# Kernel optimization log

Measured on AMD Instinct MI355X. Metric: run time of the kernel, lower is better.

Reference implementation:

```python
import jax, jax.numpy as jnp
import numpy as np

KERNEL_MUL = 2.0
KERNEL_NUM = 5


def setup_inputs() -> dict:
    key = jax.random.key(0)
    k1, k2 = jax.random.split(key)
    N, D = 4096, 256
    source = jax.random.normal(k1, (N, D), dtype=jnp.float32)
    target = jax.random.normal(k2, (N, D), dtype=jnp.float32)
    return {"source": source, "target": target}


def _gaussian_kernel_sum(source, target):
    # total: [2N, D]
    total = jnp.concatenate([source, target], axis=0)
    n = total.shape[0]
    sq = jnp.sum(total * total, axis=1)  # [2N]
    L2 = sq[:, None] + sq[None, :] - 2.0 * (total @ total.T)  # [2N, 2N]
    # Bandwidth from detached mean of off-diagonal-normalized sum (torch uses .data)
    bandwidth = jax.lax.stop_gradient(jnp.sum(L2)) / (n * n - n)
    bandwidth = bandwidth / (KERNEL_MUL ** (KERNEL_NUM // 2))
    kernels = sum(
        jnp.exp(-L2 / (bandwidth * (KERNEL_MUL ** i))) for i in range(KERNEL_NUM)
    )
    return kernels


def reference(source, target):
    b = source.shape[0]
    K = _gaussian_kernel_sum(source, target)
    XX = jnp.mean(K[:b, :b])
    YY = jnp.mean(K[b:, b:])
    XY = jnp.mean(K[:b, b:])
    YX = jnp.mean(K[b:, :b])
    return XX + YY - XY - YX
```

## Files before the change

kernel.cpp:

```cpp
#include <hip/hip_runtime.h>


#define NROWS 8192
#define HALF  4096
#define DIM   256
#define CONVB 256
#define NTILE 2080

typedef float f32x4 __attribute__((ext_vector_type(4)));

__device__ __forceinline__ const float* row_ptr(const float* src, const float* tgt, int r) {
    return (r < HALF) ? (src + (size_t)r * DIM) : (tgt + (size_t)(r - HALF) * DIM);
}

__global__ __launch_bounds__(256) void k_conv(const float* __restrict__ src,
                                              const float* __restrict__ tgt,
                                              unsigned char* __restrict__ hi,
                                              float* __restrict__ sq,
                                              float* __restrict__ part,
                                              double* __restrict__ parts1,
                                              float* __restrict__ out) {
    __shared__ __align__(16) unsigned char sh8[32 * 256];
    __shared__ float4 cs[4][64];
    __shared__ double s1s[4];

    int w = threadIdx.x >> 6, lane = threadIdx.x & 63;
    int r0 = blockIdx.x * 32;

    float4 v[8];
    #pragma unroll
    for (int i = 0; i < 8; ++i) {
        int row = r0 + w * 8 + i;
        v[i] = ((const float4*)row_ptr(src, tgt, row))[lane];
    }

    float4 csum = {0.f, 0.f, 0.f, 0.f};
    double s1w = 0.0;
    #pragma unroll
    for (int i = 0; i < 8; ++i) {
        int rl  = w * 8 + i;
        float xs[4] = {v[i].x, v[i].y, v[i].z, v[i].w};
        int pk = __builtin_amdgcn_cvt_pk_fp8_f32(xs[0], xs[1], 0, false);
        pk     = __builtin_amdgcn_cvt_pk_fp8_f32(xs[2], xs[3], pk, true);
        int o  = lane >> 1, h = lane & 1;
        *(int*)&sh8[rl * 256 + (((o ^ rl) & 31) << 3) + (h << 2)] = pk;
        csum.x += xs[0]; csum.y += xs[1]; csum.z += xs[2]; csum.w += xs[3];
        float sf = xs[0]*xs[0] + xs[1]*xs[1] + xs[2]*xs[2] + xs[3]*xs[3];
        float q0 = __builtin_amdgcn_cvt_f32_fp8(pk, 0);
        float q1 = __builtin_amdgcn_cvt_f32_fp8(pk, 1);
        float q2 = __builtin_amdgcn_cvt_f32_fp8(pk, 2);
        float q3 = __builtin_amdgcn_cvt_f32_fp8(pk, 3);
        float sQ = q0*q0 + q1*q1 + q2*q2 + q3*q3;
        #pragma unroll
        for (int off = 32; off; off >>= 1) {
            sf += __shfl_xor(sf, off, 64);
            sQ += __shfl_xor(sQ, off, 64);
        }
        if (lane == 0) { sq[r0 + rl] = sQ; s1w += (double)sf; }
    }
    __syncthreads();
    int panel = blockIdx.x >> 2, quarter = blockIdx.x & 3;
    #pragma unroll
    for (int c = threadIdx.x; c < 512; c += 256) {
        int u = c >> 5, rl = c & 31;
        int tt = u >> 2, j = u & 3;
        int o0 = 8 * tt + j;
        int o1 = 8 * tt + 4 + j;
        unsigned long long q0 = *(const unsigned long long*)
            &sh8[rl * 256 + (((o0 ^ rl) & 31) << 3)];
        unsigned long long q1 = *(const unsigned long long*)
            &sh8[rl * 256 + (((o1 ^ rl) & 31) << 3)];
        ulonglong2 q = {q0, q1};
        size_t goff = ((size_t)panel * 2048 + (size_t)u * 128 + quarter * 32 + rl);
        ((ulonglong2*)hi)[goff] = q;
    }
    cs[w][lane] = csum;
    if (lane == 0) s1s[w] = s1w;
    __syncthreads();
    if (w == 0) {
        float4 a = cs[0][lane], b = cs[1][lane], c = cs[2][lane], d = cs[3][lane];
        float4 tot = {a.x + b.x + c.x + d.x, a.y + b.y + c.y + d.y,
                      a.z + b.z + c.z + d.z, a.w + b.w + c.w + d.w};
        *(float4*)&part[(size_t)blockIdx.x * DIM + lane * 4] = tot;
        if (lane == 0) parts1[blockIdx.x] = s1s[0] + s1s[1] + s1s[2] + s1s[3];
    }
    if (blockIdx.x == 0 && threadIdx.x == 0) out[0] = 0.0f;
}

__global__ __launch_bounds__(256) void k_scale(const double* __restrict__ parts1,
                                               const float* __restrict__ part,
                                               float* __restrict__ scale) {
    __shared__ double sh[256];
    int t = threadIdx.x;
    sh[t] = parts1[t];
    __syncthreads();
    for (int off = 128; off; off >>= 1) {
        if (t < off) sh[t] += sh[t + off];
        __syncthreads();
    }
    double S1 = sh[0];
    __syncthreads();
    float c0 = 0.f, c1 = 0.f, c2 = 0.f, c3 = 0.f;
    #pragma unroll 16
    for (int b = 0; b < CONVB; b += 4) {
        c0 += part[(b + 0) * DIM + t];
        c1 += part[(b + 1) * DIM + t];
        c2 += part[(b + 2) * DIM + t];
        c3 += part[(b + 3) * DIM + t];
    }
    double c = (double)((c0 + c1) + (c2 + c3));
    sh[t] = c * c;
    __syncthreads();
    for (int off = 128; off; off >>= 1) {
        if (t < off) sh[t] += sh[t + off];
        __syncthreads();
    }
    if (t == 0) {
        double S2    = sh[0];
        double n     = (double)NROWS;
        double sumL2 = 2.0 * n * S1 - 2.0 * S2;
        double bw    = sumL2 / (n * n - n) / 4.0;
        *scale = (float)(-1.0 / (16.0 * bw * 0.69314718055994530942));
    }
}

__global__ __launch_bounds__(256, 2) void k_pairs(const unsigned char* __restrict__ hi,
                                                  const float* __restrict__ sq,
                                                  const float* __restrict__ scale_p,
                                                  float* __restrict__ out) {
    int id = blockIdx.x;
    int I = 0;
    for (;;) {
        int cnt = 64 - I;
        if (id < cnt) break;
        id -= cnt; ++I;
    }
    int J = I + id;

    __shared__ float wsum[4];

    int t    = threadIdx.x;
    int lane = t & 63;
    int w    = t >> 6;
    int lr   = lane & 15, lq = lane >> 4;
    int wr   = w >> 1, wc = w & 1;

    float wgt = (J == I) ? 1.0f : 2.0f;
    float sgn = ((I < 32) == (J < 32)) ? 1.0f : -1.0f;

    const ulonglong2* hp = (const ulonglong2*)hi;
    const ulonglong2* pA = hp + (size_t)I * 2048 + (size_t)lq * 128 + wr * 64 + lr;
    const ulonglong2* pB = hp + (size_t)J * 2048 + (size_t)lq * 128 + wc * 64 + lr;

    f32x4 acc[4][4];
    #pragma unroll
    for (int m = 0; m < 4; ++m)
        #pragma unroll
        for (int n = 0; n < 4; ++n) acc[m][n] = (f32x4){0.f, 0.f, 0.f, 0.f};

    ulonglong2 fA[4][4], fB[4][4];
    #pragma unroll
    for (int tt = 0; tt < 4; ++tt) {
        #pragma unroll
        for (int m = 0; m < 4; ++m) fA[tt][m] = pA[tt * 512 + m * 16];
        #pragma unroll
        for (int n = 0; n < 4; ++n) fB[tt][n] = pB[tt * 512 + n * 16];
    }

    #pragma unroll
    for (int tt = 0; tt < 4; ++tt) {
        #pragma unroll
        for (int m = 0; m < 4; ++m)
            #pragma unroll
            for (int n = 0; n < 4; ++n)
                acc[m][n] = __builtin_amdgcn_mfma_f32_16x16x32_fp8_fp8(
                    (long)fA[tt][m].x, (long)fB[tt][n].x, acc[m][n], 0, 0, 0);
        #pragma unroll
        for (int m = 0; m < 4; ++m)
            #pragma unroll
            for (int n = 0; n < 4; ++n)
                acc[m][n] = __builtin_amdgcn_mfma_f32_16x16x32_fp8_fp8(
                    (long)fA[tt][m].y, (long)fB[tt][n].y, acc[m][n], 0, 0, 0);
    }

    float scale = *scale_p;
    int ro_eff = I * 128 + wr * 64;
    int co_eff = J * 128 + wc * 64;
    float4 sqa4[4];
    float  sqbv[4];
    #pragma unroll
    for (int m = 0; m < 4; ++m) sqa4[m] = *(const float4*)&sq[ro_eff + m * 16 + lq * 4];
    #pragma unroll
    for (int n = 0; n < 4; ++n) sqbv[n] = sq[co_eff + n * 16 + lr];

    float tsum = 0.0f;
    #pragma unroll
    for (int m = 0; m < 4; ++m) {
        float sa[4] = {sqa4[m].x, sqa4[m].y, sqa4[m].z, sqa4[m].w};
        #pragma unroll
        for (int n = 0; n < 4; ++n) {
            #pragma unroll
            for (int r = 0; r < 4; ++r) {
                float L2  = sa[r] + sqbv[n] - 2.0f * acc[m][n][r];
                float u   = __builtin_amdgcn_exp2f(scale * L2);
                float u2  = u * u;
                float u4  = u2 * u2;
                float u8  = u4 * u4;
                float u16 = u8 * u8;
                tsum += u + u2 + u4 + u8 + u16;
            }
        }
    }

    #pragma unroll
    for (int off = 32; off; off >>= 1) tsum += __shfl_xor(tsum, off, 64);
    if (lane == 0) wsum[w] = tsum;
    __syncthreads();
    if (t == 0) {
        float tot = wsum[0] + wsum[1] + wsum[2] + wsum[3];
        atomicAdd(out, tot * sgn * wgt * (1.0f / ((float)HALF * (float)HALF)));
    }
}

extern "C" void kernel_launch(void* const* d_in, const int* in_sizes, int n_in,
                              void* d_out, int out_size, void* d_ws, size_t ws_size,
                              hipStream_t stream) {
    const float* src = (const float*)d_in[0];
    const float* tgt = (const float*)d_in[1];
    float* out = (float*)d_out;

    char* ws = (char*)d_ws;
    float*  scale  = (float*)(ws + 16);
    float*  sq     = (float*)(ws + 64);
    float*  part   = (float*)(ws + 64 + 32768);
    double* parts1 = (double*)(ws + 64 + 32768 + 262144);
    unsigned char* hi = (unsigned char*)(ws + 297024);

    k_conv <<<CONVB, 256, 0, stream>>>(src, tgt, hi, sq, part, parts1, out);
    k_scale<<<1, 256, 0, stream>>>(parts1, part, scale);
    k_pairs<<<NTILE, 256, 0, stream>>>(hi, sq, scale, out);
}
```

Baseline: 104.6 us.

## Stage fp8 operand panels into LDS via direct global-to-LDS loads

k_pairs now copies the A and B fp8 panels into shared memory with global_load_lds DMA instructions and XOR-swizzled addresses, then reads MFMA fragments from LDS per k-step. Previously every wave loaded its fragments straight from global memory, so data was duplicated across waves and all fragments sat in registers at once. Diagonal tiles load only one panel. This lowers register pressure and redundant global traffic, but adds 64KB of LDS per block, which may cut occupancy, and adds a full wait and barrier before compute.

```diff
diff --git a/kernel.cpp b/kernel.cpp
--- a/kernel.cpp
+++ b/kernel.cpp
@@ -11,6 +11,12 @@
 
 __device__ __forceinline__ const float* row_ptr(const float* src, const float* tgt, int r) {
     return (r < HALF) ? (src + (size_t)r * DIM) : (tgt + (size_t)(r - HALF) * DIM);
+}
+
+__device__ __forceinline__ void gload_lds16(const void* g, void* l) {
+    __builtin_amdgcn_global_load_lds(
+        (const __attribute__((address_space(1))) unsigned int*)g,
+        (__attribute__((address_space(3))) unsigned int*)l, 16, 0, 0);
 }
 
 __global__ __launch_bounds__(256) void k_conv(const float* __restrict__ src,
@@ -128,6 +134,10 @@
                                                   const float* __restrict__ sq,
                                                   const float* __restrict__ scale_p,
                                                   float* __restrict__ out) {
+    __shared__ __align__(16) ulonglong2 ldsA[2048];
+    __shared__ __align__(16) ulonglong2 ldsB[2048];
+    __shared__ float wsum[4];
+
     int id = blockIdx.x;
     int I = 0;
     for (;;) {
@@ -137,8 +147,6 @@
     }
     int J = I + id;
 
-    __shared__ float wsum[4];
-
     int t    = threadIdx.x;
     int lane = t & 63;
     int w    = t >> 6;
@@ -148,9 +156,27 @@
     float wgt = (J == I) ? 1.0f : 2.0f;
     float sgn = ((I < 32) == (J < 32)) ? 1.0f : -1.0f;
 
-    const ulonglong2* hp = (const ulonglong2*)hi;
-    const ulonglong2* pA = hp + (size_t)I * 2048 + (size_t)lq * 128 + wr * 64 + lr;
-    const ulonglong2* pB = hp + (size_t)J * 2048 + (size_t)lq * 128 + wc * 64 + lr;
+    const ulonglong2* plane = (const ulonglong2*)hi;
+    int nIns = (J == I) ? 32 : 64;
+    for (int i = 0; i < 16; ++i) {
+        int k = w + 4 * i;
+        if (k >= nIns) break;
+        int p  = k >> 5;
+        int u  = (k >> 1) & 15;
+        int h  = k & 1;
+        int rg = (h * 64 + lane) ^ ((u & 3) << 1);
+        size_t gUnit = (size_t)(p ? J : I) * 2048 + (size_t)u * 128 + rg;
+        ulonglong2* ldst = (p ? ldsB : ldsA) + (u * 128 + h * 64);
+        gload_lds16(plane + gUnit, ldst);
+    }
+    asm volatile("s_waitcnt vmcnt(0)");
+    __syncthreads();
+
+    const ulonglong2* lA = ldsA;
+    const ulonglong2* lB = (J == I) ? ldsA : ldsB;
+    int lrx = lr ^ (lq << 1);
+    const ulonglong2* pAl = lA + lq * 128 + wr * 64 + lrx;
+    const ulonglong2* pBl = lB + lq * 128 + wc * 64 + lrx;
 
     f32x4 acc[4][4];
     #pragma unroll
@@ -158,29 +184,25 @@
         #pragma unroll
         for (int n = 0; n < 4; ++n) acc[m][n] = (f32x4){0.f, 0.f, 0.f, 0.f};
 
-    ulonglong2 fA[4][4], fB[4][4];
     #pragma unroll
     for (int tt = 0; tt < 4; ++tt) {
-        #pragma unroll
-        for (int m = 0; m < 4; ++m) fA[tt][m] = pA[tt * 512 + m * 16];
-        #pragma unroll
-        for (int n = 0; n < 4; ++n) fB[tt][n] = pB[tt * 512 + n * 16];
-    }
-
-    #pragma unroll
-    for (int tt = 0; tt < 4; ++tt) {
+        ulonglong2 fA[4], fB[4];
+        #pragma unroll
+        for (int m = 0; m < 4; ++m) fA[m] = pAl[tt * 512 + m * 16];
+        #pragma unroll
+        for (int n = 0; n < 4; ++n) fB[n] = pBl[tt * 512 + n * 16];
         #pragma unroll
         for (int m = 0; m < 4; ++m)
             #pragma unroll
             for (int n = 0; n < 4; ++n)
                 acc[m][n] = __builtin_amdgcn_mfma_f32_16x16x32_fp8_fp8(
-                    (long)fA[tt][m].x, (long)fB[tt][n].x, acc[m][n], 0, 0, 0);
+                    (long)fA[m].x, (long)fB[n].x, acc[m][n], 0, 0, 0);
         #pragma unroll
         for (int m = 0; m < 4; ++m)
             #pragma unroll
             for (int n = 0; n < 4; ++n)
                 acc[m][n] = __builtin_amdgcn_mfma_f32_16x16x32_fp8_fp8(
-                    (long)fA[tt][m].y, (long)fB[tt][n].y, acc[m][n], 0, 0, 0);
+                    (long)fA[m].y, (long)fB[n].y, acc[m][n], 0, 0, 0);
     }
 
     float scale = *scale_p;
```

Measured after the change: 103.4 us. No clear change (-1.1%).
